# Optimization experiments

Hardware: AMD Instinct MI355X
Metric: run time of the kernel (lower is better)

Reference implementation:

```python
import jax, jax.numpy as jnp
import numpy as np

NUM_BITS = 2
QN = -(2 ** (NUM_BITS - 1))          # -2 (signed)
QP = 2 ** (NUM_BITS - 1) - 1         # 1
NUM_LEVELS = 2 ** NUM_BITS           # 4


def setup_inputs() -> dict:
    key = jax.random.key(0)
    k1, k2 = jax.random.split(key)
    # Large transformer FFN weight matrix: d_model=4096, d_ff=16384
    weights = jax.random.normal(k1, (4096, 16384), dtype=jnp.float32) * 0.1
    alpha = jax.random.uniform(k2, (1,), dtype=jnp.float32, minval=0.05, maxval=0.2)
    return {"weights": weights, "alpha": alpha}


def reference(weights, alpha):
    # backprop_to_alpha=False -> alpha is detached everywhere (torch uses .item())
    a = jax.lax.stop_gradient(alpha[0])
    w = weights.reshape(-1)

    # LSQ quantization levels: [Qn*a, ..., -a, 0, a, ..., Qp*a]
    levels = jnp.arange(QN, QP + 1, dtype=w.dtype) * a            # [NUM_LEVELS]

    # Bin assignment by LSQ integer code (non-differentiable indices)
    bins = jnp.round(jnp.clip(w / a, QN, QP)).astype(jnp.int32)   # in [QN, QP]
    idx = bins - QN                                               # in [0, NUM_LEVELS)

    # Single-pass per-bin sum / sumsq / count (replaces per-bin mask loop)
    count = jax.ops.segment_sum(jnp.ones_like(w), idx, num_segments=NUM_LEVELS)
    s = jax.ops.segment_sum(w, idx, num_segments=NUM_LEVELS)
    sq = jax.ops.segment_sum(w * w, idx, num_segments=NUM_LEVELS)

    safe = jnp.maximum(count, 1.0)
    mean = s / safe
    var = sq / safe - mean * mean                                 # biased (unbiased=False)

    total_mse = jnp.sum(jnp.where(count > 0, (mean - levels) ** 2, 0.0))
    total_var = jnp.sum(jnp.where(count >= 2, var, 0.0))
    loss = total_mse + total_var

    # Diagnostics (computed under no_grad in torch)
    wq = bins.astype(w.dtype) * a                                 # quantized weights
    d = jax.lax.stop_gradient(w - wq)
    mean_distance = jnp.mean(jnp.abs(d))
    quantization_mse = jnp.mean(d * d)

    return jnp.stack([loss, total_mse, total_var, quantization_mse, mean_distance])
```

## Files before the change

### kernel.cpp

```cpp
#include <hip/hip_runtime.h>
#include <cstdint>

#define TS 16384
#define NSLOT 13
#define NCH 7
#define NW 4096


__device__ __forceinline__ int kbin_th(float x, double T1, double T2) {
    double xd = (double)x;
    if (xd >   T1) return 1;
    if (xd >= -T1) return 0;
    if (xd >  -T2) return -1;
    return -2;
}

__device__ __forceinline__ double wred64(double v) {
#pragma unroll
    for (int d = 32; d >= 1; d >>= 1) v += __shfl_xor(v, d, 64);
    return v;
}
__device__ __forceinline__ int wred32i(int v) {
#pragma unroll
    for (int d = 32; d >= 1; d >>= 1) v += __shfl_xor(v, d, 64);
    return v;
}

__device__ __forceinline__ int expo_bits(double A) {
    const long long b = __double_as_longlong(A);
    return (int)((b >> 52) & 0x7FF) - 1023;
}
__device__ __forceinline__ int emin_of(double A0) {
    if (!(A0 > 0.0)) return 12345;
    const int e = expo_bits(A0);
    if (e < -100 || e > 100) return 12345;
    return e;
}

__global__ __launch_bounds__(64) void zero2(double* __restrict__ diag,
        float* __restrict__ chains, double* __restrict__ A0d) {
    if (threadIdx.x < 8) {
        diag[threadIdx.x] = 0.0;
        chains[threadIdx.x] = 0.0f;
        A0d[threadIdx.x] = 0.0;
    }
}

__global__ __launch_bounds__(256) void part1(const float* __restrict__ w,
        const float* __restrict__ alpha, int* __restrict__ hist,
        double* __restrict__ dpart, long long n, long long nsegw)
{
    const float a = alpha[0];
    const double T1 = (double)a * (0.5 + 0x1p-25);
    const double T2 = (double)a * (1.5 - 0x1p-24);
    const int wv = threadIdx.x >> 6, lane = threadIdx.x & 63;
    const int sid = blockIdx.x * 4 + wv;
    const long long seg = (long long)sid * nsegw;
    long long send = seg + nsegw; if (send > n) send = n;
    int h0=0,h1=0,h2=0,h3=0;
    double ad=0.0, dd=0.0, s0=0.0;

    for (long long base = seg; base < send; base += 256) {
        const long long i = base + (long long)lane * 4;
        if (i >= send) break;
        float4 v;
        if (i + 3 < send) v = *reinterpret_cast<const float4*>(w + i);
        else {
            v = make_float4(0.f,0.f,0.f,0.f);
            v.x = w[i];
            if (i+1 < send) v.y = w[i+1];
            if (i+2 < send) v.z = w[i+2];
        }
        const float xs[4] = {v.x, v.y, v.z, v.w};
        const int nv = (int)((send - i) < 4 ? (send - i) : 4);
#pragma unroll
        for (int j = 0; j < 4; ++j) {
            if (j >= nv) break;
            const float x = xs[j];
            const int k = kbin_th(x, T1, T2);
            h0 += (k==-2); h1 += (k==-1); h2 += (k==0); h3 += (k==1);
            const float bf = (float)k;
            const float wq = __fmul_rn(bf, a);
            const float d  = __fsub_rn(x, wq);
            ad += (double)fabsf(d);
            dd += (double)__fmul_rn(d, d);
            if (k == 0) s0 += (double)x;
        }
    }

    h0 = wred32i(h0); h1 = wred32i(h1); h2 = wred32i(h2); h3 = wred32i(h3);
    ad = wred64(ad);  dd = wred64(dd);  s0 = wred64(s0);

    if (lane == 0) {
        hist[sid*4 + 0] = h0;
        hist[sid*4 + 1] = h1;
        hist[sid*4 + 2] = h2;
        hist[sid*4 + 3] = h3;
        dpart[sid*4 + 0] = ad;
        dpart[sid*4 + 1] = dd;
        dpart[sid*4 + 2] = s0;
    }
}

__global__ __launch_bounds__(256) void scank(const int* __restrict__ hist,
        const double* __restrict__ dpart, int* __restrict__ bbase,
        int* __restrict__ hdr, double* __restrict__ diag)
{
    const int wv = threadIdx.x >> 6, lane = threadIdx.x & 63;
    if (wv < 4) {
        int running = 0;
        for (int c = 0; c < NW/64; ++c) {
            int v = hist[(c*64 + lane)*4 + wv];
            int p = v;
#pragma unroll
            for (int d = 1; d < 64; d <<= 1) {
                int t = __shfl_up(p, d, 64);
                if (lane >= d) p += t;
            }
            bbase[(c*64+lane)*4 + wv] = running + p - v;
            running += __shfl(p, 63, 64);
        }
        if (lane == 0) hdr[wv] = running;
    }
    __syncthreads();
    if (threadIdx.x == 0) {
        int b = 0;
        for (int q = 0; q < 4; ++q) { hdr[4+q] = b; b += (hdr[q] + 63) & ~63; }
    }

    double a0=0.0, a1=0.0, a2=0.0;
    for (int e = threadIdx.x; e < NW; e += 256) {
        a0 += dpart[e*4+0]; a1 += dpart[e*4+1]; a2 += dpart[e*4+2];
    }
    a0 = wred64(a0); a1 = wred64(a1); a2 = wred64(a2);
    __shared__ double dsh[4][3];
    if (lane == 0) { dsh[wv][0]=a0; dsh[wv][1]=a1; dsh[wv][2]=a2; }
    __syncthreads();
    if (threadIdx.x == 0) {
        diag[0] = dsh[0][0]+dsh[1][0]+dsh[2][0]+dsh[3][0];
        diag[1] = dsh[0][1]+dsh[1][1]+dsh[2][1]+dsh[3][1];
        diag[2] = dsh[0][2]+dsh[1][2]+dsh[2][2]+dsh[3][2];
    }
}

__global__ __launch_bounds__(256) void part2(const float* __restrict__ w,
        const float* __restrict__ alpha, const int* __restrict__ bbase,
        const int* __restrict__ hdr, float* __restrict__ streams,
        long long n, long long nsegw)
{
    const float a = alpha[0];
    const double T1 = (double)a * (0.5 + 0x1p-25);
    const double T2 = (double)a * (1.5 - 0x1p-24);
    const int wv = threadIdx.x >> 6, lane = threadIdx.x & 63;
    const int sid = blockIdx.x * 4 + wv;
    const unsigned long long ltmask = (1ULL << lane) - 1ULL;

    int run0 = hdr[4+0] + bbase[sid*4 + 0];
    int run1 = hdr[4+1] + bbase[sid*4 + 1];
    int run2 = hdr[4+2] + bbase[sid*4 + 2];
    int run3 = hdr[4+3] + bbase[sid*4 + 3];

    const long long seg = (long long)sid * nsegw;
    long long send = seg + nsegw; if (send > n) send = n;

    for (long long base = seg; base < send; base += 256) {
        const long long i = base + (long long)lane * 4;
        float xs[4]; int kk[4];
        if (i + 3 < send) {
            const float4 v = *reinterpret_cast<const float4*>(w + i);
            xs[0]=v.x; xs[1]=v.y; xs[2]=v.z; xs[3]=v.w;
            kk[0]=kbin_th(xs[0],T1,T2); kk[1]=kbin_th(xs[1],T1,T2);
            kk[2]=kbin_th(xs[2],T1,T2); kk[3]=kbin_th(xs[3],T1,T2);
        } else {
#pragma unroll
            for (int j = 0; j < 4; ++j) {
                const long long idx = i + j;
                if (idx < send) { xs[j] = w[idx]; kk[j] = kbin_th(xs[j],T1,T2); }
                else            { xs[j] = 0.f;   kk[j] = 9; }
            }
        }

        int br0=0,br1=0,br2=0,br3=0;
        int tt0=0,tt1=0,tt2=0,tt3=0;
#pragma unroll
        for (int j = 0; j < 4; ++j) {
            const unsigned long long b0 = __ballot(kk[j] == -2);
            const unsigned long long b1 = __ballot(kk[j] == -1);
            const unsigned long long b2 = __ballot(kk[j] ==  0);
            const unsigned long long b3 = __ballot(kk[j] ==  1);
            br0 += __popcll(b0 & ltmask); tt0 += __popcll(b0);
            br1 += __popcll(b1 & ltmask); tt1 += __popcll(b1);
            br2 += __popcll(b2 & ltmask); tt2 += __popcll(b2);
            br3 += __popcll(b3 & ltmask); tt3 += __popcll(b3);
        }

        int own0=0, own1=0, own2=0, own3=0;
#pragma unroll
        for (int j = 0; j < 4; ++j) {
            const int k = kk[j];
            if      (k == -2) { streams[(long long)(run0 + br0 + own0)] = xs[j]; ++own0; }
            else if (k == -1) { streams[(long long)(run1 + br1 + own1)] = xs[j]; ++own1; }
            else if (k ==  0) { streams[(long long)(run2 + br2 + own2)] = xs[j]; ++own2; }
            else if (k ==  1) { streams[(long long)(run3 + br3 + own3)] = xs[j]; ++own3; }
        }
        run0 += tt0; run1 += tt1; run2 += tt2; run3 += tt3;
    }
}

__device__ void span_st(const float* __restrict__ p, int isq,
                        double& A, long long lo, long long hi, int lane)
{
    for (long long base = lo; base < hi; base += 4096) {
        float xs[64];
        const long long e0 = base + (long long)lane * 64;
#pragma unroll
        for (int q4 = 0; q4 < 16; ++q4) {
            const long long fi = e0 + q4 * 4;
            float4 v = make_float4(0.f,0.f,0.f,0.f);
            if (fi + 3 < hi) v = *reinterpret_cast<const float4*>(p + fi);
            else {
                if (fi     < hi) v.x = p[fi];
                if (fi + 1 < hi) v.y = p[fi + 1];
                if (fi + 2 < hi) v.z = p[fi + 2];
            }
            xs[q4*4+0]=v.x; xs[q4*4+1]=v.y; xs[q4*4+2]=v.z; xs[q4*4+3]=v.w;
        }
#pragma unroll
        for (int j = 0; j < 64; ++j) {
            const float x = xs[j];
            xs[j] = isq ? __fmul_rn(x, x) : fabsf(x);
        }

        int C = 0;
        while (C < 64) {
            if (A > 0.0) {
                const int e = ilogb(A);
                const double u  = ldexp(1.0, e - 23);
                const double Bb = ldexp(1.0, e + 1);
                const double sc = ldexp(1.0, 23 - e);
                double kd = 0.0;
                if (lane >= C) {
#pragma unroll
                    for (int j = 0; j < 64; ++j) kd += rint((double)xs[j] * sc);
                }
                const bool big = kd >= 1099511627776.0;
                double pp = kd;
#pragma unroll
                for (int d = 1; d < 64; d <<= 1) {
                    double tt = __shfl_up(pp, d, 64);
                    if (lane >= d) pp += tt;
                }
                const bool cross = (lane >= C) && (big || (A + u * pp >= Bb));
                const unsigned long long bal = __ballot(cross);
                if (bal == 0ULL) {
                    A = A + u * __shfl(pp, 63);
                    break;
                }
                const int F = __ffsll((long long)bal) - 1;
                double An = 0.0;
                if (lane == F) {
                    const double Aex = A + u * (pp - kd);
                    float Af = (float)Aex;
#pragma unroll
                    for (int j = 0; j < 64; ++j) Af = __fadd_rn(Af, xs[j]);
                    An = (double)Af;
                }
                A = __shfl(An, F);
                C = F + 1;
            } else {
                bool has = false;
                if (lane >= C) {
#pragma unroll
                    for (int j = 0; j < 64; ++j) has = has || (xs[j] > 0.0f);
                }
                const unsigned long long bal = __ballot(has);
                if (bal == 0ULL) break;
                const int F = __ffsll((long long)bal) - 1;
                double An = 0.0;
                if (lane == F) {
                    float Af = 0.0f;
#pragma unroll
                    for (int j = 0; j < 64; ++j) Af = __fadd_rn(Af, xs[j]);
                    An = (double)Af;
                }
                A = __shfl(An, F);
                C = F + 1;
            }
        }
    }
}

__global__ __launch_bounds__(64) void span0(const float* __restrict__ streams,
        const int* __restrict__ hdr, double* __restrict__ A0d)
{
    const int ch = blockIdx.x;
    const int STR[NCH] = {0,1,3,0,1,2,3};
    const int ISQ[NCH] = {0,0,0,1,1,1,1};
    const int st = STR[ch];
    const long long cnt = (long long)hdr[st];
    const float* p = streams + hdr[4+st];
    double A = 0.0;
    if (cnt > 0)
        span_st(p, ISQ[ch], A, 0LL, (TS < cnt ? (long long)TS : cnt), threadIdx.x);
    if (threadIdx.x == 0) A0d[ch] = A;
}

template<int HASS>
__device__ __forceinline__ void passA_two(const float* __restrict__ p,
        long long cnt, double* __restrict__ krowS, double* __restrict__ krowQ,
        float baseS, float baseQ, long long ntg, long long tile)
{
    const long long lo = tile * TS;
    long long hi = lo + TS; if (hi > cnt) hi = cnt;

    float scS[NSLOT], scQ[NSLOT];
    scS[0] = baseS; scQ[0] = baseQ;
#pragma unroll
    for (int s = 1; s < NSLOT; ++s) { scS[s] = scS[s-1]*0.5f; scQ[s] = scQ[s-1]*0.5f; }
    int accS[NSLOT], accQ[NSLOT];
#pragma unroll
    for (int s = 0; s < NSLOT; ++s) { accS[s] = 0; accQ[s] = 0; }

    const int tid = threadIdx.x;
    for (long long i = lo + (long long)tid*4; i < hi; i += 256*4) {
        float4 v;
        if (i + 3 < hi) v = *reinterpret_cast<const float4*>(p + i);
        else {
            v = make_float4(0.f,0.f,0.f,0.f);
            v.x = p[i];
            if (i+1 < hi) v.y = p[i+1];
            if (i+2 < hi) v.z = p[i+2];
        }
        const float xsv[4] = {v.x, v.y, v.z, v.w};
#pragma unroll
        for (int j = 0; j < 4; ++j) {
            const float x  = xsv[j];
            const float xq = __fmul_rn(x, x);
            if (HASS) {
                const float ax = fabsf(x);
#pragma unroll
                for (int s = 0; s < NSLOT; ++s)
                    accS[s] += (int)rintf(ax * scS[s]);
            }
#pragma unroll
            for (int s = 0; s < NSLOT; ++s)
                accQ[s] += (int)rintf(xq * scQ[s]);
        }
    }

    __shared__ double lred[4][2*NSLOT];
    const int lane = tid & 63, wv = tid >> 6;
#pragma unroll
    for (int s = 0; s < NSLOT; ++s) {
        double rs = wred64((double)accS[s]);
        double rq = wred64((double)accQ[s]);
        if (lane == 0) { lred[wv][s] = rs; lred[wv][NSLOT+s] = rq; }
    }
    __syncthreads();
    if (tid < 2*NSLOT) {
        const double sum = lred[0][tid]+lred[1][tid]+lred[2][tid]+lred[3][tid];
        if (tid < NSLOT) {
            if (HASS) krowS[(long long)tid * ntg + tile] = sum;
        } else {
            krowQ[(long long)(tid-NSLOT) * ntg + tile] = sum;
        }
    }
}

__global__ __launch_bounds__(256) void passA7(const float* __restrict__ streams,
        const int* __restrict__ hdr, const double* __restrict__ A0d,
        double* __restrict__ Ktab, long long ntg)
{
    const int st = blockIdx.y;
    const int SCH[4] = {0, 1, -1, 2};
    const int QCH[4] = {3, 4,  5, 6};
    const long long cnt = (long long)hdr[st];
    const long long tile = blockIdx.x;
    if (tile * TS >= cnt) return;
    const float* p = streams + hdr[4+st];

    const int qch = QCH[st];
    const int emQ = emin_of(A0d[qch]);
    const float baseQ = (emQ == 12345) ? 0.0f : ldexpf(1.0f, 23 - emQ);
    double* krowQ = Ktab + (long long)qch * NSLOT * ntg;

    if (SCH[st] >= 0) {
        const int sch = SCH[st];
        const int emS = emin_of(A0d[sch]);
        const float baseS = (emS == 12345) ? 0.0f : ldexpf(1.0f, 23 - emS);
        double* krowS = Ktab + (long long)sch * NSLOT * ntg;
        passA_two<1>(p, cnt, krowS, krowQ, baseS, baseQ, ntg, tile);
    } else {
        passA_two<0>(p, cnt, nullptr, krowQ, 0.0f, baseQ, ntg, tile);
    }
}

__global__ __launch_bounds__(64) void walk2(const float* __restrict__ streams,
        const int* __restrict__ hdr, const double* __restrict__ A0d,
        const double* __restrict__ Ktab, float* __restrict__ chains, long long ntg)
{
    const int ch = blockIdx.x;
    const int lane = threadIdx.x;
    const int STR[NCH]  = {0,1,3,0,1,2,3};
    const int ISQ[NCH]  = {0,0,0,1,1,1,1};
    const int OSLOT[NCH]= {0,1,3,4,5,6,7};
    const int st = STR[ch], isq = ISQ[ch];
    const long long cnt = (long long)hdr[st];
    const float* p = streams + hdr[4+st];
    const long long ntiles = (cnt + TS - 1) / TS;
    const double* krow = Ktab + (long long)ch * NSLOT * ntg;
    const int em = emin_of(A0d[ch]);

    double A = A0d[ch];
    long long t = 1;
    while (t < ntiles) {
        if (A > 0.0 && em != 12345) {
            const int e = expo_bits(A);
            const int slot = e - em;
            if (slot >= 0 && slot < NSLOT) {
                const long long wt = t + lane;
                double Kv = (wt < ntiles) ? krow[(long long)slot * ntg + wt] : 0.0;
                double P = Kv;
#pragma unroll
                for (int d = 1; d < 64; d <<= 1) {
                    double tt = __shfl_up(P, d, 64);
                    if (lane >= d) P += tt;
                }
                const double u  = ldexp(1.0, e - 23);
                const double Bb = ldexp(1.0, e + 1);
                const bool bad = (A + u * P > Bb);
                const unsigned long long bal = __ballot(bad);
                if (bal == 0ULL) { A += u * __shfl(P, 63); t += 64; continue; }
                const int F = __ffsll((long long)bal) - 1;
                if (F > 0) { A += u * __shfl(P, F - 1); t += F; }
                const long long lo = t * (long long)TS;
                long long hi = lo + TS; if (hi > cnt) hi = cnt;
                span_st(p, isq, A, lo, hi, lane);
                ++t;
                continue;
            }
        }
        const long long lo = t * (long long)TS;
        long long hi = lo + TS; if (hi > cnt) hi = cnt;
        span_st(p, isq, A, lo, hi, lane);
        ++t;
    }
    if (lane == 0) chains[OSLOT[ch]] = (float)A;
}

__global__ void fin2(const float* __restrict__ chains,
                     const double* __restrict__ diag,
                     const int* __restrict__ hdr,
                     const float* __restrict__ alpha,
                     float* __restrict__ out, long long n)
{
    const float a = alpha[0];
    const float s_np[4]  = { -chains[0], -chains[1], (float)diag[2], chains[3] };
    const float sq_np[4] = {  chains[4],  chains[5],  chains[6],     chains[7] };
    float tmse = 0.f, tvar = 0.f;
#pragma unroll
    for (int b = 0; b < 4; ++b) {
        float cnt = fminf((float)hdr[b], 16777216.0f);
        float safe = fmaxf(cnt, 1.0f);
        float mean = __fdiv_rn(s_np[b], safe);
        float var  = __fsub_rn(__fdiv_rn(sq_np[b], safe), __fmul_rn(mean, mean));
        float lvl  = __fmul_rn((float)(b - 2), a);
        float e    = __fsub_rn(mean, lvl);
        if (cnt > 0.f)  tmse = __fadd_rn(tmse, __fmul_rn(e, e));
        if (cnt >= 2.f) tvar = __fadd_rn(tvar, var);
    }
    out[0] = __fadd_rn(tmse, tvar);
    out[1] = tmse;
    out[2] = tvar;
    out[3] = (float)(diag[1] / (double)n);
    out[4] = (float)(diag[0] / (double)n);
}

__global__ __launch_bounds__(64) void zero_diag6(double* __restrict__ diag) {
    if (threadIdx.x < 6) diag[threadIdx.x] = 0.0;
}
__global__ __launch_bounds__(256) void diag6(const float* __restrict__ w,
        const float* __restrict__ alpha, double* __restrict__ diag, int n4, long long n)
{
    const float a = alpha[0];
    float ad = 0.f, dd = 0.f; int c0=0,c1=0,c2=0,c3=0;
    auto pe = [&](float x) {
        float r = __fdiv_rn(x, a);
        float cl = fminf(1.0f, fmaxf(-2.0f, r));
        float bf = rintf(cl); int k = (int)bf;
        float wq = __fmul_rn(bf, a); float d = __fsub_rn(x, wq);
        ad = __fadd_rn(ad, fabsf(d)); dd = __fadd_rn(dd, __fmul_rn(d, d));
        if (k==-2) c0++; else if (k==-1) c1++; else if (k==0) c2++; else c3++;
    };
    const float4* w4 = reinterpret_cast<const float4*>(w);
    const int stride = gridDim.x * 256;
    for (int i = blockIdx.x * 256 + threadIdx.x; i < n4; i += stride) {
        float4 v = w4[i]; pe(v.x); pe(v.y); pe(v.z); pe(v.w);
    }
    if (blockIdx.x == 0 && threadIdx.x == 0)
        for (long long i = (long long)n4 * 4; i < n; ++i) pe(w[i]);
    double vals[6] = {(double)ad,(double)dd,(double)c0,(double)c1,(double)c2,(double)c3};
    __shared__ double red[256];
    const int tid = threadIdx.x;
#pragma unroll
    for (int j = 0; j < 6; ++j) {
        red[tid] = vals[j]; __syncthreads();
        for (int s = 128; s > 0; s >>= 1) { if (tid < s) red[tid] += red[tid+s]; __syncthreads(); }
        if (tid == 0) atomicAdd(&diag[j], red[0]);
        __syncthreads();
    }
}
__global__ __launch_bounds__(64) void seq_chains(const float* __restrict__ w,
        const float* __restrict__ alpha, float* __restrict__ chains, long long n)
{
    const float a = alpha[0];
    const int lane = threadIdx.x; const int myrow = lane & 7;
    __shared__ float val[8][64];
    float acc = 0.0f;
    const long long ntl = (n + 63) / 64;
    float x_next = (lane < n) ? w[lane] : 0.0f;
    for (long long t = 0; t < ntl; ++t) {
        float x = x_next;
        { long long idxn = (t + 1) * 64 + lane; x_next = (idxn < n) ? w[idxn] : 0.0f; }
        const long long idx = t * 64 + lane;
        const bool valid = (idx < n);
        float r = __fdiv_rn(x, a);
        float cl = fminf(1.0f, fmaxf(-2.0f, r));
        int k = (int)rintf(cl); int row = k + 2;
        float xx = __fmul_rn(x, x);
#pragma unroll
        for (int b = 0; b < 4; ++b) {
            val[b][lane]     = (valid && row == b) ? x  : 0.0f;
            val[4 + b][lane] = (valid && row == b) ? xx : 0.0f;
        }
        __syncthreads();
        if (lane < 8) {
#pragma unroll
            for (int e4i = 0; e4i < 16; ++e4i) {
                float4 v = *reinterpret_cast<const float4*>(&val[myrow][e4i * 4]);
                acc = __fadd_rn(acc, v.x); acc = __fadd_rn(acc, v.y);
                acc = __fadd_rn(acc, v.z); acc = __fadd_rn(acc, v.w);
            }
        }
        __syncthreads();
    }
    if (lane < 8) chains[lane] = acc;
}
__global__ void fin_seq(const float* __restrict__ chains, const double* __restrict__ diag,
                        const float* __restrict__ alpha, float* __restrict__ out, long long n)
{
    const float a = alpha[0];
    float tmse = 0.0f, tvar = 0.0f;
#pragma unroll
    for (int b = 0; b < 4; ++b) {
        float cnt = fminf((float)diag[2 + b], 16777216.0f);
        float safe = fmaxf(cnt, 1.0f);
        float mean = __fdiv_rn(chains[b], safe);
        float var  = __fsub_rn(__fdiv_rn(chains[4 + b], safe), __fmul_rn(mean, mean));
        float lvl  = __fmul_rn((float)(b - 2), a);
        float e    = __fsub_rn(mean, lvl);
        if (cnt > 0.0f)  tmse = __fadd_rn(tmse, __fmul_rn(e, e));
        if (cnt >= 2.0f) tvar = __fadd_rn(tvar, var);
    }
    out[0] = __fadd_rn(tmse, tvar);
    out[1] = tmse; out[2] = tvar;
    out[3] = (float)(diag[1] / (double)n);
    out[4] = (float)(diag[0] / (double)n);
}

extern "C" void kernel_launch(void* const* d_in, const int* in_sizes, int n_in,
                              void* d_out, int out_size, void* d_ws, size_t ws_size,
                              hipStream_t stream) {
    const float* w     = (const float*)d_in[0];
    const float* alpha = (const float*)d_in[1];
    float* out = (float*)d_out;
    const long long n = (long long)in_sizes[0];
    const long long ntg = (n + TS - 1) / TS;

    size_t off = 0;
    const size_t ktab_off = off;   off += (size_t)NCH * NSLOT * ntg * 8;
    const size_t hist_off = off;   off += (size_t)NW * 4 * 4;
    const size_t bbase_off = off;  off += (size_t)NW * 4 * 4;
    const size_t hdr_off = off;    off += 8 * 4;
    const size_t diag_off = (off + 7) & ~(size_t)7;  off = diag_off + 8 * 8;
    const size_t dpart_off = off;  off += (size_t)NW * 4 * 8;
    const size_t a0_off = off;     off += 8 * 8;
    const size_t chains_off = off; off += 8 * 4;
    const size_t streams_off = (off + 255) & ~(size_t)255;
    const size_t need1 = streams_off + ((size_t)n + 512) * 4;

    if (ws_size >= need1) {
        double* Ktab   = (double*)((char*)d_ws + ktab_off);
        int*    hist   = (int*)   ((char*)d_ws + hist_off);
        int*    bbase  = (int*)   ((char*)d_ws + bbase_off);
        int*    hdr    = (int*)   ((char*)d_ws + hdr_off);
        double* diag   = (double*)((char*)d_ws + diag_off);
        double* dpart  = (double*)((char*)d_ws + dpart_off);
        double* A0d    = (double*)((char*)d_ws + a0_off);
        float*  chains = (float*) ((char*)d_ws + chains_off);
        float*  strm   = (float*) ((char*)d_ws + streams_off);
        long long nsegw = ((n + NW - 1) / NW + 255) & ~255LL;

        zero2<<<1, 64, 0, stream>>>(diag, chains, A0d);
        part1<<<NW/4, 256, 0, stream>>>(w, alpha, hist, dpart, n, nsegw);
        scank<<<1, 256, 0, stream>>>(hist, dpart, bbase, hdr, diag);
        part2<<<NW/4, 256, 0, stream>>>(w, alpha, bbase, hdr, strm, n, nsegw);
        span0<<<NCH, 64, 0, stream>>>(strm, hdr, A0d);
        dim3 ga((unsigned)ntg, 4);
        passA7<<<ga, 256, 0, stream>>>(strm, hdr, A0d, Ktab, ntg);
        walk2<<<NCH, 64, 0, stream>>>(strm, hdr, A0d, Ktab, chains, ntg);
        fin2<<<1, 1, 0, stream>>>(chains, diag, hdr, alpha, out, n);
    } else {
        float*  chains = (float*)d_ws;
        double* diag   = (double*)((char*)d_ws + 128);
        zero_diag6<<<1, 64, 0, stream>>>(diag);
        diag6<<<1024, 256, 0, stream>>>(w, alpha, diag, (int)(n >> 2), n);
        seq_chains<<<1, 64, 0, stream>>>(w, alpha, chains, n);
        fin_seq<<<1, 1, 0, stream>>>(chains, diag, alpha, out, n);
    }
}
```

Measured before the change: 575.5 us.

## Use float bin thresholds, float accumulators, 128-wide walk scan, drop zero kernel

Replaces the double-precision bin thresholds with exact float bounds, found by a per-thread bisection against the rounded division, so classification uses float compares. The passA histogram-slot accumulators switch from int conversion to float adds. The walk kernel now does a two-wavefront prefix scan so it can skip 128 tiles per step. The zero2 launch is removed, which saves a tiny kernel. Risks include float accumulator precision loss in passA, bisection overhead in every thread, and dependence on buffers that are no longer zeroed first.

```diff
diff --git a/kernel.cpp b/kernel.cpp
--- a/kernel.cpp
+++ b/kernel.cpp
@@ -7,11 +7,27 @@
 #define NW 4096
 
 
-__device__ __forceinline__ int kbin_th(float x, double T1, double T2) {
-    double xd = (double)x;
-    if (xd >   T1) return 1;
-    if (xd >= -T1) return 0;
-    if (xd >  -T2) return -1;
+__device__ __forceinline__ void f32_bounds(float a, float& B1, float& B2) {
+    unsigned lo = __float_as_uint(__fmul_rn(a, 0.49f));
+    unsigned hi = __float_as_uint(__fmul_rn(a, 0.51f));
+    while (hi - lo > 1u) {
+        const unsigned mid = lo + ((hi - lo) >> 1);
+        if (__fdiv_rn(__uint_as_float(mid), a) <= 0.5f) lo = mid; else hi = mid;
+    }
+    B1 = __uint_as_float(lo);
+    lo = __float_as_uint(__fmul_rn(a, 1.49f));
+    hi = __float_as_uint(__fmul_rn(a, 1.51f));
+    while (hi - lo > 1u) {
+        const unsigned mid = lo + ((hi - lo) >> 1);
+        if (__fdiv_rn(__uint_as_float(mid), a) < 1.5f) lo = mid; else hi = mid;
+    }
+    B2 = __uint_as_float(hi);
+}
+
+__device__ __forceinline__ int kbin_f(float x, float B1, float B2) {
+    if (x >   B1) return 1;
+    if (x >= -B1) return 0;
+    if (x >  -B2) return -1;
     return -2;
 }
 
@@ -37,22 +53,13 @@
     return e;
 }
 
-__global__ __launch_bounds__(64) void zero2(double* __restrict__ diag,
-        float* __restrict__ chains, double* __restrict__ A0d) {
-    if (threadIdx.x < 8) {
-        diag[threadIdx.x] = 0.0;
-        chains[threadIdx.x] = 0.0f;
-        A0d[threadIdx.x] = 0.0;
-    }
-}
-
 __global__ __launch_bounds__(256) void part1(const float* __restrict__ w,
         const float* __restrict__ alpha, int* __restrict__ hist,
         double* __restrict__ dpart, long long n, long long nsegw)
 {
     const float a = alpha[0];
-    const double T1 = (double)a * (0.5 + 0x1p-25);
-    const double T2 = (double)a * (1.5 - 0x1p-24);
+    float B1, B2;
+    f32_bounds(a, B1, B2);
     const int wv = threadIdx.x >> 6, lane = threadIdx.x & 63;
     const int sid = blockIdx.x * 4 + wv;
     const long long seg = (long long)sid * nsegw;
@@ -77,7 +84,7 @@
         for (int j = 0; j < 4; ++j) {
             if (j >= nv) break;
             const float x = xs[j];
-            const int k = kbin_th(x, T1, T2);
+            const int k = kbin_f(x, B1, B2);
             h0 += (k==-2); h1 += (k==-1); h2 += (k==0); h3 += (k==1);
             const float bf = (float)k;
             const float wq = __fmul_rn(bf, a);
@@ -149,8 +156,8 @@
         long long n, long long nsegw)
 {
     const float a = alpha[0];
-    const double T1 = (double)a * (0.5 + 0x1p-25);
-    const double T2 = (double)a * (1.5 - 0x1p-24);
+    float B1, B2;
+    f32_bounds(a, B1, B2);
     const int wv = threadIdx.x >> 6, lane = threadIdx.x & 63;
     const int sid = blockIdx.x * 4 + wv;
     const unsigned long long ltmask = (1ULL << lane) - 1ULL;
@@ -169,13 +176,13 @@
         if (i + 3 < send) {
             const float4 v = *reinterpret_cast<const float4*>(w + i);
             xs[0]=v.x; xs[1]=v.y; xs[2]=v.z; xs[3]=v.w;
-            kk[0]=kbin_th(xs[0],T1,T2); kk[1]=kbin_th(xs[1],T1,T2);
-            kk[2]=kbin_th(xs[2],T1,T2); kk[3]=kbin_th(xs[3],T1,T2);
+            kk[0]=kbin_f(xs[0],B1,B2); kk[1]=kbin_f(xs[1],B1,B2);
+            kk[2]=kbin_f(xs[2],B1,B2); kk[3]=kbin_f(xs[3],B1,B2);
         } else {
 #pragma unroll
             for (int j = 0; j < 4; ++j) {
                 const long long idx = i + j;
-                if (idx < send) { xs[j] = w[idx]; kk[j] = kbin_th(xs[j],T1,T2); }
+                if (idx < send) { xs[j] = w[idx]; kk[j] = kbin_f(xs[j],B1,B2); }
                 else            { xs[j] = 0.f;   kk[j] = 9; }
             }
         }
@@ -317,9 +324,9 @@
     scS[0] = baseS; scQ[0] = baseQ;
 #pragma unroll
     for (int s = 1; s < NSLOT; ++s) { scS[s] = scS[s-1]*0.5f; scQ[s] = scQ[s-1]*0.5f; }
-    int accS[NSLOT], accQ[NSLOT];
-#pragma unroll
-    for (int s = 0; s < NSLOT; ++s) { accS[s] = 0; accQ[s] = 0; }
+    float accS[NSLOT], accQ[NSLOT];
+#pragma unroll
+    for (int s = 0; s < NSLOT; ++s) { accS[s] = 0.f; accQ[s] = 0.f; }
 
     const int tid = threadIdx.x;
     for (long long i = lo + (long long)tid*4; i < hi; i += 256*4) {
@@ -340,11 +347,11 @@
                 const float ax = fabsf(x);
 #pragma unroll
                 for (int s = 0; s < NSLOT; ++s)
-                    accS[s] += (int)rintf(ax * scS[s]);
+                    accS[s] += rintf(ax * scS[s]);
             }
 #pragma unroll
             for (int s = 0; s < NSLOT; ++s)
-                accQ[s] += (int)rintf(xq * scQ[s]);
+                accQ[s] += rintf(xq * scQ[s]);
         }
     }
 
@@ -418,21 +425,41 @@
             const int e = expo_bits(A);
             const int slot = e - em;
             if (slot >= 0 && slot < NSLOT) {
-                const long long wt = t + lane;
-                double Kv = (wt < ntiles) ? krow[(long long)slot * ntg + wt] : 0.0;
-                double P = Kv;
+                const long long wt0 = t + lane;
+                const long long wt1 = t + 64 + lane;
+                double Kv0 = (wt0 < ntiles) ? krow[(long long)slot * ntg + wt0] : 0.0;
+                double Kv1 = (wt1 < ntiles) ? krow[(long long)slot * ntg + wt1] : 0.0;
+                double P0 = Kv0;
 #pragma unroll
                 for (int d = 1; d < 64; d <<= 1) {
-                    double tt = __shfl_up(P, d, 64);
-                    if (lane >= d) P += tt;
-                }
+                    double tt = __shfl_up(P0, d, 64);
+                    if (lane >= d) P0 += tt;
+                }
+                const double tot0 = __shfl(P0, 63);
+                double P1 = Kv1;
+#pragma unroll
+                for (int d = 1; d < 64; d <<= 1) {
+                    double tt = __shfl_up(P1, d, 64);
+                    if (lane >= d) P1 += tt;
+                }
+                P1 += tot0;
                 const double u  = ldexp(1.0, e - 23);
                 const double Bb = ldexp(1.0, e + 1);
-                const bool bad = (A + u * P > Bb);
-                const unsigned long long bal = __ballot(bad);
-                if (bal == 0ULL) { A += u * __shfl(P, 63); t += 64; continue; }
-                const int F = __ffsll((long long)bal) - 1;
-                if (F > 0) { A += u * __shfl(P, F - 1); t += F; }
+                const unsigned long long bal0 = __ballot(A + u * P0 > Bb);
+                const unsigned long long bal1 = __ballot(A + u * P1 > Bb);
+                if (bal0 == 0ULL && bal1 == 0ULL) {
+                    A += u * __shfl(P1, 63);
+                    t += 128;
+                    continue;
+                }
+                const int F = (bal0 != 0ULL) ? (__ffsll((long long)bal0) - 1)
+                                             : (64 + __ffsll((long long)bal1) - 1);
+                if (F > 0) {
+                    const double cv = (F <= 64) ? __shfl(P0, F - 1)
+                                                : __shfl(P1, F - 65);
+                    A += u * cv;
+                    t += F;
+                }
                 const long long lo = t * (long long)TS;
                 long long hi = lo + TS; if (hi > cnt) hi = cnt;
                 span_st(p, isq, A, lo, hi, lane);
@@ -601,7 +628,6 @@
         float*  strm   = (float*) ((char*)d_ws + streams_off);
         long long nsegw = ((n + NW - 1) / NW + 255) & ~255LL;
 
-        zero2<<<1, 64, 0, stream>>>(diag, chains, A0d);
         part1<<<NW/4, 256, 0, stream>>>(w, alpha, hist, dpart, n, nsegw);
         scank<<<1, 256, 0, stream>>>(hist, dpart, bbase, hdr, diag);
         part2<<<NW/4, 256, 0, stream>>>(w, alpha, bbase, hdr, strm, n, nsegw);
```

Result: faster. 555.6 us (-3.5%).
